# Kernel tuning notes

Measured on AMD Instinct MI355X. Metric: run time of the kernel, lower is better.

Reference implementation:

```python
import jax, jax.numpy as jnp
import numpy as np

L, H, P, R = 8192, 1024, 512, 256


def setup_inputs() -> dict:
    key = jax.random.key(0)
    ks = jax.random.split(key, 12)
    nrm = lambda k, s, std=0.01: std * jax.random.normal(k, s, dtype=jnp.float32)
    # Stable complex diagonal: |Lambda_bar| in [0.8, 0.999)
    mag = 0.8 + 0.199 * jax.random.uniform(ks[8], (P,), dtype=jnp.float32)
    phase = jnp.pi * jax.random.uniform(ks[9], (P,), dtype=jnp.float32)
    return {
        "input_sequence": jax.random.normal(ks[0], (L, H), dtype=jnp.float32),
        "F": nrm(ks[1], (R, H)),
        "H_proj": nrm(ks[2], (R, H)),
        "Delta_p": jnp.eye(R, dtype=jnp.float32),
        "Delta_r": jnp.eye(R, dtype=jnp.float32),
        "E": nrm(ks[3], (P, R)),
        "G": nrm(ks[4], (H, R)),
        "Lambda_bar_re": (mag * jnp.cos(phase)).astype(jnp.float32),
        "Lambda_bar_im": (mag * jnp.sin(phase)).astype(jnp.float32),
        "B_bar_re": nrm(ks[5], (P, H), 0.05),
        "B_bar_im": nrm(ks[6], (P, H), 0.05),
        "C_re": nrm(ks[7], (H, P), 0.05),
        "C_im": nrm(ks[10], (H, P), 0.05),
        "D": nrm(ks[11], (H, H), 0.02),
    }


def _binop(a, b):
    # Diagonal linear SSM associative combine: (lam, bu)
    return (b[0] * a[0], b[0] * a[1] + b[1])


def reference(input_sequence, F, H_proj, Delta_p, Delta_r, E, G,
              Lambda_bar_re, Lambda_bar_im, B_bar_re, B_bar_im,
              C_re, C_im, D):
    # p_k = Delta_p @ (F @ u_k), r_k = Delta_r @ (H_proj @ u_k)  -- vmapped over L via matmul
    p_seq = (input_sequence @ F.T) @ Delta_p.T            # (L, R)
    r_seq = (input_sequence @ H_proj.T) @ Delta_r.T       # (L, R)
    up_seq = jnp.concatenate([input_sequence, p_seq], axis=-1)  # (L, H+R)

    Lam = (Lambda_bar_re + 1j * Lambda_bar_im).astype(jnp.complex64)         # (P,)
    B_bar = (B_bar_re + 1j * B_bar_im).astype(jnp.complex64)                 # (P, H)
    B_ext = jnp.concatenate([B_bar, E.astype(jnp.complex64)], axis=1)        # (P, H+R)

    # Per-step driving term Bu_k = B_ext @ up_k
    Bu = up_seq.astype(jnp.complex64) @ B_ext.T                               # (L, P)
    Lam_el = jnp.broadcast_to(Lam, Bu.shape)                                  # (L, P)

    # Parallel associative scan: x_k = Lam * x_{k-1} + Bu_k
    _, xs = jax.lax.associative_scan(_binop, (Lam_el, Bu))                    # (L, P)

    C_tilde = (C_re + 1j * C_im).astype(jnp.complex64)                        # (H, P)
    # conj_sym=True branch: y_k = 2*Re(C_tilde @ x_k) + G @ r_k + D @ u_k
    y_seq = (2.0 * jnp.real(xs @ C_tilde.T)
             + r_seq @ G.T
             + input_sequence @ D.T)                                           # (L, H)
    return y_seq
```

## Files before the change

kernel.cpp:

```cpp
#include <hip/hip_runtime.h>
#include <stdint.h>

#define L_SEQ 8192
#define HDIM  1024
#define PDIM  512
#define RDIM  256
#define NCHUNK 64
#define CHUNK  128

typedef __attribute__((ext_vector_type(8))) short bf16x8;
typedef __attribute__((ext_vector_type(4))) float f32x4;
typedef __attribute__((ext_vector_type(4))) int   i32x4;

__device__ inline unsigned short f2bf(float x) {
  unsigned u = __builtin_bit_cast(unsigned, x);
  unsigned r = (u + 0x7fffu + ((u >> 16) & 1u)) >> 16;
  return (unsigned short)r;
}

__global__ __launch_bounds__(256) void transpose_cast(const float* __restrict__ src,
                                                      unsigned short* __restrict__ dst,
                                                      int R, int Hd) {
  __shared__ float tile[32][33];
  int bx = blockIdx.x * 32;
  int by = blockIdx.y * 32;
  int tx = threadIdx.x, ty = threadIdx.y;
#pragma unroll
  for (int dy = 0; dy < 32; dy += 8)
    tile[ty + dy][tx] = src[(size_t)(by + ty + dy) * Hd + bx + tx];
  __syncthreads();
#pragma unroll
  for (int dy = 0; dy < 32; dy += 8)
    dst[(size_t)(bx + ty + dy) * R + by + tx] = f2bf(tile[tx][ty + dy]);
}

__global__ __launch_bounds__(256) void cast_flat(const float* __restrict__ src,
                                                 unsigned short* __restrict__ dst,
                                                 int n4, float scale) {
  int g = blockIdx.x * 256 + threadIdx.x;
  if (g >= n4) return;
  float4 v = *(const float4*)(src + (size_t)g * 4);
  ushort4 o;
  o.x = f2bf(v.x * scale); o.y = f2bf(v.y * scale);
  o.z = f2bf(v.z * scale); o.w = f2bf(v.w * scale);
  *(ushort4*)(dst + (size_t)g * 4) = o;
}

__global__ __launch_bounds__(256) void cast_strided(const float* __restrict__ src, int ldsrc,
                                                    unsigned short* __restrict__ dst, int lddst,
                                                    int rows, int cols, float scale) {
  int g = blockIdx.x * 256 + threadIdx.x;
  int c4 = cols >> 2;
  int total = rows * c4;
  if (g >= total) return;
  int row = g / c4;
  int c = (g - row * c4) * 4;
  float4 v = *(const float4*)(src + (size_t)row * ldsrc + c);
  ushort4 o;
  o.x = f2bf(v.x * scale); o.y = f2bf(v.y * scale);
  o.z = f2bf(v.z * scale); o.w = f2bf(v.w * scale);
  *(ushort4*)(dst + (size_t)row * lddst + c) = o;
}

template <int HAS_ADD, int OUT_F32, int OUT_BF16>
__global__ __launch_bounds__(256) void gemm_bt(const unsigned short* __restrict__ A, int lda,
                                               const unsigned short* __restrict__ B, int ldb,
                                               float* __restrict__ C, int ldc,
                                               unsigned short* __restrict__ Cb, int ldcb,
                                               const float* __restrict__ Add, int ldadd,
                                               int K) {
  __shared__ __align__(16) unsigned short sA[128 * 32];
  __shared__ __align__(16) unsigned short sB[128 * 32];
  const int m0 = blockIdx.x * 128, n0 = blockIdx.y * 128;
  const int tid = threadIdx.x;
  const int lane = tid & 63, wave = tid >> 6;
  const int wm = wave >> 1, wn = wave & 1;
  const int frow = lane & 15, fg = lane >> 4;

  f32x4 acc[4][4] = {};

  for (int kt = 0; kt < K; kt += 32) {
    i32x4 ra[2], rb[2];
#pragma unroll
    for (int it = 0; it < 2; ++it) {
      int flat = it * 256 + tid;
      int r = flat >> 2, c8 = (flat & 3) * 8;
      ra[it] = *(const i32x4*)(A + (size_t)(m0 + r) * lda + kt + c8);
      rb[it] = *(const i32x4*)(B + (size_t)(n0 + r) * ldb + kt + c8);
    }
    __syncthreads();
#pragma unroll
    for (int it = 0; it < 2; ++it) {
      int flat = it * 256 + tid;
      int r = flat >> 2, c8 = (flat & 3) * 8;
      *(i32x4*)(sA + r * 32 + c8) = ra[it];
      *(i32x4*)(sB + r * 32 + c8) = rb[it];
    }
    __syncthreads();
    bf16x8 fa[4], fb[4];
#pragma unroll
    for (int f = 0; f < 4; ++f) {
      fa[f] = *(const bf16x8*)(sA + (wm * 64 + f * 16 + frow) * 32 + fg * 8);
      fb[f] = *(const bf16x8*)(sB + (wn * 64 + f * 16 + frow) * 32 + fg * 8);
    }
#pragma unroll
    for (int i = 0; i < 4; ++i)
#pragma unroll
      for (int j = 0; j < 4; ++j)
        acc[i][j] = __builtin_amdgcn_mfma_f32_16x16x32_bf16(fa[i], fb[j], acc[i][j], 0, 0, 0);
  }

  const int crow4 = (lane >> 4) * 4, ccol = lane & 15;
#pragma unroll
  for (int i = 0; i < 4; ++i)
#pragma unroll
    for (int j = 0; j < 4; ++j)
#pragma unroll
      for (int q = 0; q < 4; ++q) {
        int r = m0 + wm * 64 + i * 16 + crow4 + q;
        int c = n0 + wn * 64 + j * 16 + ccol;
        float v = acc[i][j][q];
        if (HAS_ADD) v += Add[(size_t)r * ldadd + c];
        if (OUT_F32) C[(size_t)r * ldc + c] = v;
        if (OUT_BF16) Cb[(size_t)r * ldcb + c] = f2bf(v);
      }
}

__global__ __launch_bounds__(256) void scan_carry(const float* __restrict__ Bu,
                                                  const float* __restrict__ lre,
                                                  const float* __restrict__ lim,
                                                  float* __restrict__ carry) {
  int g = blockIdx.x * 256 + threadIdx.x;
  int p = g & 511, c = g >> 9;
  float ar = lre[p], ai = lim[p];
  float sr = 0.f, si = 0.f;
  const float* base = Bu + (size_t)c * CHUNK * 1024 + p;
#pragma unroll 4
  for (int i = 0; i < CHUNK; ++i) {
    float br = base[(size_t)i * 1024];
    float bi = base[(size_t)i * 1024 + 512];
    float nr = ar * sr - ai * si + br;
    float ni = ar * si + ai * sr + bi;
    sr = nr; si = ni;
  }
  carry[c * 512 + p] = sr;
  carry[NCHUNK * 512 + c * 512 + p] = si;
}

__global__ __launch_bounds__(512) void scan_prefix(const float* __restrict__ carry,
                                                   const float* __restrict__ lre,
                                                   const float* __restrict__ lim,
                                                   float* __restrict__ prefix) {
  int p = threadIdx.x;
  float ar = lre[p], ai = lim[p];
  float cr = ar, ci = ai;
#pragma unroll
  for (int s = 0; s < 7; ++s) {
    float t = cr * cr - ci * ci;
    ci = 2.f * cr * ci;
    cr = t;
  }
  float sr = 0.f, si = 0.f;
  for (int c = 0; c < NCHUNK; ++c) {
    float br = carry[c * 512 + p], bi = carry[NCHUNK * 512 + c * 512 + p];
    float nr = cr * sr - ci * si + br;
    float ni = cr * si + ci * sr + bi;
    sr = nr; si = ni;
    prefix[c * 512 + p] = sr;
    prefix[NCHUNK * 512 + c * 512 + p] = si;
  }
}

__global__ __launch_bounds__(256) void scan_apply(const float* __restrict__ Bu,
                                                  const float* __restrict__ lre,
                                                  const float* __restrict__ lim,
                                                  const float* __restrict__ prefix,
                                                  unsigned short* __restrict__ A2) {
  int g = blockIdx.x * 256 + threadIdx.x;
  int p = g & 511, c = g >> 9;
  float ar = lre[p], ai = lim[p];
  float sr = 0.f, si = 0.f;
  if (c > 0) {
    sr = prefix[(c - 1) * 512 + p];
    si = prefix[NCHUNK * 512 + (c - 1) * 512 + p];
  }
  const float* base = Bu + (size_t)c * CHUNK * 1024 + p;
  unsigned short* ob = A2 + (size_t)c * CHUNK * 2048 + 1024 + p;
#pragma unroll 4
  for (int i = 0; i < CHUNK; ++i) {
    float br = base[(size_t)i * 1024];
    float bi = base[(size_t)i * 1024 + 512];
    float nr = ar * sr - ai * si + br;
    float ni = ar * si + ai * sr + bi;
    sr = nr; si = ni;
    ob[(size_t)i * 2048] = f2bf(sr);
    ob[(size_t)i * 2048 + 512] = f2bf(si);
  }
}

extern "C" void kernel_launch(void* const* d_in, const int* in_sizes, int n_in,
                              void* d_out, int out_size, void* d_ws, size_t ws_size,
                              hipStream_t stream) {
  const float* u   = (const float*)d_in[0];
  const float* F   = (const float*)d_in[1];
  const float* Hp  = (const float*)d_in[2];
  const float* dP  = (const float*)d_in[3];
  const float* dR  = (const float*)d_in[4];
  const float* E   = (const float*)d_in[5];
  const float* G   = (const float*)d_in[6];
  const float* lre = (const float*)d_in[7];
  const float* lim = (const float*)d_in[8];
  const float* Bre = (const float*)d_in[9];
  const float* Bim = (const float*)d_in[10];
  const float* Cre = (const float*)d_in[11];
  const float* Cim = (const float*)d_in[12];
  const float* Dm  = (const float*)d_in[13];
  float* y = (float*)d_out;

  uint8_t* ws = (uint8_t*)d_ws;
  size_t off = 0;
  auto alloc = [&](size_t bytes) {
    void* p = ws + off;
    off += (bytes + 255) & ~(size_t)255;
    return p;
  };
  unsigned short* A2  = (unsigned short*)alloc((size_t)L_SEQ * 2048 * 2);
  unsigned short* W1  = (unsigned short*)alloc((size_t)1024 * 1024 * 2);
  unsigned short* Wy  = (unsigned short*)alloc((size_t)1024 * 2048 * 2);
  float*          Bu  = (float*)alloc((size_t)L_SEQ * 1024 * 4);
  unsigned short* Ft  = (unsigned short*)alloc((size_t)1024 * 256 * 2);
  unsigned short* Ht  = (unsigned short*)alloc((size_t)1024 * 256 * 2);
  unsigned short* FpT = (unsigned short*)alloc((size_t)1024 * 256 * 2);
  unsigned short* HrT = (unsigned short*)alloc((size_t)1024 * 256 * 2);
  unsigned short* dPb = (unsigned short*)alloc((size_t)256 * 256 * 2);
  unsigned short* dRb = (unsigned short*)alloc((size_t)256 * 256 * 2);
  unsigned short* Eb  = (unsigned short*)alloc((size_t)512 * 256 * 2);
  unsigned short* Gb  = (unsigned short*)alloc((size_t)1024 * 256 * 2);
  float* carry  = (float*)alloc((size_t)2 * NCHUNK * 512 * 4);
  float* prefix = (float*)alloc((size_t)2 * NCHUNK * 512 * 4);
  (void)ws_size; (void)in_sizes; (void)n_in; (void)out_size;

  transpose_cast<<<dim3(32, 8), dim3(32, 8), 0, stream>>>(F, Ft, 256, 1024);
  transpose_cast<<<dim3(32, 8), dim3(32, 8), 0, stream>>>(Hp, Ht, 256, 1024);
  cast_flat<<<(65536 / 4 + 255) / 256, 256, 0, stream>>>(dP, dPb, 65536 / 4, 1.f);
  cast_flat<<<(65536 / 4 + 255) / 256, 256, 0, stream>>>(dR, dRb, 65536 / 4, 1.f);
  cast_flat<<<(131072 / 4 + 255) / 256, 256, 0, stream>>>(E, Eb, 131072 / 4, 1.f);
  cast_flat<<<(262144 / 4 + 255) / 256, 256, 0, stream>>>(G, Gb, 262144 / 4, 1.f);
  cast_strided<<<((L_SEQ * 256) + 255) / 256, 256, 0, stream>>>(u, 1024, A2, 2048, L_SEQ, 1024, 1.f);
  cast_flat<<<((512 * 1024 / 4) + 255) / 256, 256, 0, stream>>>(Bim, W1 + (size_t)512 * 1024, 512 * 1024 / 4, 1.f);
  cast_strided<<<((1024 * 128) + 255) / 256, 256, 0, stream>>>(Cre, 512, Wy + 1024, 2048, 1024, 512, 2.f);
  cast_strided<<<((1024 * 128) + 255) / 256, 256, 0, stream>>>(Cim, 512, Wy + 1536, 2048, 1024, 512, -2.f);

  gemm_bt<0, 0, 1><<<dim3(8, 2), 256, 0, stream>>>(Ft, 256, dPb, 256, nullptr, 0, FpT, 256, nullptr, 0, 256);
  gemm_bt<0, 0, 1><<<dim3(8, 2), 256, 0, stream>>>(Ht, 256, dRb, 256, nullptr, 0, HrT, 256, nullptr, 0, 256);
  gemm_bt<1, 0, 1><<<dim3(4, 8), 256, 0, stream>>>(Eb, 256, FpT, 256, nullptr, 0, W1, 1024, Bre, 1024, 256);
  gemm_bt<1, 0, 1><<<dim3(8, 8), 256, 0, stream>>>(Gb, 256, HrT, 256, nullptr, 0, Wy, 2048, Dm, 1024, 256);

  gemm_bt<0, 1, 0><<<dim3(64, 8), 256, 0, stream>>>(A2, 2048, W1, 1024, Bu, 1024, nullptr, 0, nullptr, 0, 1024);

  scan_carry<<<128, 256, 0, stream>>>(Bu, lre, lim, carry);
  scan_prefix<<<1, 512, 0, stream>>>(carry, lre, lim, prefix);
  scan_apply<<<128, 256, 0, stream>>>(Bu, lre, lim, prefix, A2);

  gemm_bt<0, 1, 0><<<dim3(64, 8), 256, 0, stream>>>(A2, 2048, Wy, 2048, y, 1024, nullptr, 0, nullptr, 0, 2048);
}
```

Measured before the change: 286.9 us.

## Fuse prep casts into one kernel, batch small GEMMs, use direct global-to-LDS loads

All ten cast and transpose launches are merged into a single prep kernel, and the four small weight GEMMs are paired into two launches using a z-indexed dual-parameter kernel. The GEMM mainloop now loads tiles straight from global memory into LDS with global_load_lds instead of staging through registers. The scan carry and prefix buffers move to a per-channel interleaved float2 layout, and the prefix loop is batched. The goal is lower launch overhead and less register and LDS traffic. The cost is an uncoalesced strided transpose inside prep and a GEMM loop that still has no double buffering.

```diff
diff --git a/kernel.cpp b/kernel.cpp
--- a/kernel.cpp
+++ b/kernel.cpp
@@ -2,15 +2,11 @@
 #include <stdint.h>
 
 #define L_SEQ 8192
-#define HDIM  1024
-#define PDIM  512
-#define RDIM  256
 #define NCHUNK 64
 #define CHUNK  128
 
 typedef __attribute__((ext_vector_type(8))) short bf16x8;
 typedef __attribute__((ext_vector_type(4))) float f32x4;
-typedef __attribute__((ext_vector_type(4))) int   i32x4;
 
 __device__ inline unsigned short f2bf(float x) {
   unsigned u = __builtin_bit_cast(unsigned, x);
@@ -18,84 +14,114 @@
   return (unsigned short)r;
 }
 
-__global__ __launch_bounds__(256) void transpose_cast(const float* __restrict__ src,
-                                                      unsigned short* __restrict__ dst,
-                                                      int R, int Hd) {
-  __shared__ float tile[32][33];
-  int bx = blockIdx.x * 32;
-  int by = blockIdx.y * 32;
-  int tx = threadIdx.x, ty = threadIdx.y;
-#pragma unroll
-  for (int dy = 0; dy < 32; dy += 8)
-    tile[ty + dy][tx] = src[(size_t)(by + ty + dy) * Hd + bx + tx];
-  __syncthreads();
-#pragma unroll
-  for (int dy = 0; dy < 32; dy += 8)
-    dst[(size_t)(bx + ty + dy) * R + by + tx] = f2bf(tile[tx][ty + dy]);
-}
-
-__global__ __launch_bounds__(256) void cast_flat(const float* __restrict__ src,
-                                                 unsigned short* __restrict__ dst,
-                                                 int n4, float scale) {
-  int g = blockIdx.x * 256 + threadIdx.x;
-  if (g >= n4) return;
-  float4 v = *(const float4*)(src + (size_t)g * 4);
-  ushort4 o;
-  o.x = f2bf(v.x * scale); o.y = f2bf(v.y * scale);
-  o.z = f2bf(v.z * scale); o.w = f2bf(v.w * scale);
-  *(ushort4*)(dst + (size_t)g * 4) = o;
-}
-
-__global__ __launch_bounds__(256) void cast_strided(const float* __restrict__ src, int ldsrc,
-                                                    unsigned short* __restrict__ dst, int lddst,
-                                                    int rows, int cols, float scale) {
-  int g = blockIdx.x * 256 + threadIdx.x;
-  int c4 = cols >> 2;
-  int total = rows * c4;
-  if (g >= total) return;
-  int row = g / c4;
-  int c = (g - row * c4) * 4;
-  float4 v = *(const float4*)(src + (size_t)row * ldsrc + c);
-  ushort4 o;
-  o.x = f2bf(v.x * scale); o.y = f2bf(v.y * scale);
-  o.z = f2bf(v.z * scale); o.w = f2bf(v.w * scale);
-  *(ushort4*)(dst + (size_t)row * lddst + c) = o;
+#define GLD16(g, l)                                                            \
+  __builtin_amdgcn_global_load_lds(                                            \
+      (const __attribute__((address_space(1))) unsigned int*)(g),              \
+      (__attribute__((address_space(3))) unsigned int*)(l), 16, 0, 0)
+
+__global__ __launch_bounds__(256) void prep(
+    const float* __restrict__ F, const float* __restrict__ Hp,
+    const float* __restrict__ dP, const float* __restrict__ dR,
+    const float* __restrict__ E, const float* __restrict__ G,
+    const float* __restrict__ Bim, const float* __restrict__ Cre,
+    const float* __restrict__ Cim, const float* __restrict__ u,
+    unsigned short* __restrict__ Ft, unsigned short* __restrict__ Ht,
+    unsigned short* __restrict__ dPb, unsigned short* __restrict__ dRb,
+    unsigned short* __restrict__ Eb, unsigned short* __restrict__ Gb,
+    unsigned short* __restrict__ W1im, unsigned short* __restrict__ Wy,
+    unsigned short* __restrict__ A2) {
+  int q = blockIdx.x * 256 + threadIdx.x;
+  if (q < 65536) {
+    int e = q * 4, i = e >> 8, j = e & 255;
+    ushort4 o;
+    o.x = f2bf(F[(size_t)(j + 0) * 1024 + i]);
+    o.y = f2bf(F[(size_t)(j + 1) * 1024 + i]);
+    o.z = f2bf(F[(size_t)(j + 2) * 1024 + i]);
+    o.w = f2bf(F[(size_t)(j + 3) * 1024 + i]);
+    *(ushort4*)(Ft + e) = o;
+  } else if (q < 131072) {
+    int e = (q - 65536) * 4, i = e >> 8, j = e & 255;
+    ushort4 o;
+    o.x = f2bf(Hp[(size_t)(j + 0) * 1024 + i]);
+    o.y = f2bf(Hp[(size_t)(j + 1) * 1024 + i]);
+    o.z = f2bf(Hp[(size_t)(j + 2) * 1024 + i]);
+    o.w = f2bf(Hp[(size_t)(j + 3) * 1024 + i]);
+    *(ushort4*)(Ht + e) = o;
+  } else if (q < 147456) {
+    int e = (q - 131072) * 4;
+    float4 v = *(const float4*)(dP + e);
+    ushort4 o = {f2bf(v.x), f2bf(v.y), f2bf(v.z), f2bf(v.w)};
+    *(ushort4*)(dPb + e) = o;
+  } else if (q < 163840) {
+    int e = (q - 147456) * 4;
+    float4 v = *(const float4*)(dR + e);
+    ushort4 o = {f2bf(v.x), f2bf(v.y), f2bf(v.z), f2bf(v.w)};
+    *(ushort4*)(dRb + e) = o;
+  } else if (q < 196608) {
+    int e = (q - 163840) * 4;
+    float4 v = *(const float4*)(E + e);
+    ushort4 o = {f2bf(v.x), f2bf(v.y), f2bf(v.z), f2bf(v.w)};
+    *(ushort4*)(Eb + e) = o;
+  } else if (q < 262144) {
+    int e = (q - 196608) * 4;
+    float4 v = *(const float4*)(G + e);
+    ushort4 o = {f2bf(v.x), f2bf(v.y), f2bf(v.z), f2bf(v.w)};
+    *(ushort4*)(Gb + e) = o;
+  } else if (q < 393216) {
+    int e = (q - 262144) * 4;
+    float4 v = *(const float4*)(Bim + e);
+    ushort4 o = {f2bf(v.x), f2bf(v.y), f2bf(v.z), f2bf(v.w)};
+    *(ushort4*)(W1im + e) = o;
+  } else if (q < 524288) {
+    int e = (q - 393216) * 4, i = e >> 9, j = e & 511;
+    float4 v = *(const float4*)(Cre + (size_t)i * 512 + j);
+    ushort4 o = {f2bf(2.f * v.x), f2bf(2.f * v.y), f2bf(2.f * v.z), f2bf(2.f * v.w)};
+    *(ushort4*)(Wy + (size_t)i * 2048 + 1024 + j) = o;
+  } else if (q < 655360) {
+    int e = (q - 524288) * 4, i = e >> 9, j = e & 511;
+    float4 v = *(const float4*)(Cim + (size_t)i * 512 + j);
+    ushort4 o = {f2bf(-2.f * v.x), f2bf(-2.f * v.y), f2bf(-2.f * v.z), f2bf(-2.f * v.w)};
+    *(ushort4*)(Wy + (size_t)i * 2048 + 1536 + j) = o;
+  } else {
+    int e = (q - 655360) * 4, i = e >> 10, j = e & 1023;
+    float4 v = *(const float4*)(u + (size_t)i * 1024 + j);
+    ushort4 o = {f2bf(v.x), f2bf(v.y), f2bf(v.z), f2bf(v.w)};
+    *(ushort4*)(A2 + (size_t)i * 2048 + j) = o;
+  }
 }
 
 template <int HAS_ADD, int OUT_F32, int OUT_BF16>
-__global__ __launch_bounds__(256) void gemm_bt(const unsigned short* __restrict__ A, int lda,
-                                               const unsigned short* __restrict__ B, int ldb,
-                                               float* __restrict__ C, int ldc,
-                                               unsigned short* __restrict__ Cb, int ldcb,
-                                               const float* __restrict__ Add, int ldadd,
-                                               int K) {
-  __shared__ __align__(16) unsigned short sA[128 * 32];
-  __shared__ __align__(16) unsigned short sB[128 * 32];
-  const int m0 = blockIdx.x * 128, n0 = blockIdx.y * 128;
+__device__ __forceinline__ void gemm_body(
+    const unsigned short* __restrict__ A, int lda,
+    const unsigned short* __restrict__ B, int ldb,
+    float* __restrict__ C, int ldc,
+    unsigned short* __restrict__ Cb, int ldcb,
+    const float* __restrict__ Add, int ldadd, int K, int m0, int n0,
+    unsigned short* sA, unsigned short* sB) {
   const int tid = threadIdx.x;
   const int lane = tid & 63, wave = tid >> 6;
   const int wm = wave >> 1, wn = wave & 1;
   const int frow = lane & 15, fg = lane >> 4;
 
+  const int srow = lane >> 2;
+  const int scol = (lane & 3) * 8;
+  const unsigned short* gA0 = A + (size_t)(m0 + wave * 32 + srow) * lda + scol;
+  const unsigned short* gA1 = gA0 + (size_t)16 * lda;
+  const unsigned short* gB0 = B + (size_t)(n0 + wave * 32 + srow) * ldb + scol;
+  const unsigned short* gB1 = gB0 + (size_t)16 * ldb;
+  unsigned short* lA0 = sA + wave * 1024;
+  unsigned short* lA1 = lA0 + 512;
+  unsigned short* lB0 = sB + wave * 1024;
+  unsigned short* lB1 = lB0 + 512;
+
   f32x4 acc[4][4] = {};
 
   for (int kt = 0; kt < K; kt += 32) {
-    i32x4 ra[2], rb[2];
-#pragma unroll
-    for (int it = 0; it < 2; ++it) {
-      int flat = it * 256 + tid;
-      int r = flat >> 2, c8 = (flat & 3) * 8;
-      ra[it] = *(const i32x4*)(A + (size_t)(m0 + r) * lda + kt + c8);
-      rb[it] = *(const i32x4*)(B + (size_t)(n0 + r) * ldb + kt + c8);
-    }
     __syncthreads();
-#pragma unroll
-    for (int it = 0; it < 2; ++it) {
-      int flat = it * 256 + tid;
-      int r = flat >> 2, c8 = (flat & 3) * 8;
-      *(i32x4*)(sA + r * 32 + c8) = ra[it];
-      *(i32x4*)(sB + r * 32 + c8) = rb[it];
-    }
+    GLD16(gA0 + kt, lA0);
+    GLD16(gA1 + kt, lA1);
+    GLD16(gB0 + kt, lB0);
+    GLD16(gB1 + kt, lB1);
     __syncthreads();
     bf16x8 fa[4], fb[4];
 #pragma unroll
@@ -126,10 +152,44 @@
       }
 }
 
+template <int HAS_ADD, int OUT_F32, int OUT_BF16>
+__global__ __launch_bounds__(256) void gemm_bt(
+    const unsigned short* __restrict__ A, int lda,
+    const unsigned short* __restrict__ B, int ldb,
+    float* __restrict__ C, int ldc,
+    unsigned short* __restrict__ Cb, int ldcb,
+    const float* __restrict__ Add, int ldadd, int K) {
+  __shared__ __align__(16) unsigned short sA[128 * 32];
+  __shared__ __align__(16) unsigned short sB[128 * 32];
+  gemm_body<HAS_ADD, OUT_F32, OUT_BF16>(A, lda, B, ldb, C, ldc, Cb, ldcb, Add,
+                                        ldadd, K, blockIdx.x * 128,
+                                        blockIdx.y * 128, sA, sB);
+}
+
+struct GemmP {
+  const unsigned short* A; int lda;
+  const unsigned short* B; int ldb;
+  float* C; int ldc;
+  unsigned short* Cb; int ldcb;
+  const float* Add; int ldadd;
+  int K; int gx;
+};
+
+template <int HAS_ADD, int OUT_F32, int OUT_BF16>
+__global__ __launch_bounds__(256) void gemm_bt_dual(GemmP p0, GemmP p1) {
+  __shared__ __align__(16) unsigned short sA[128 * 32];
+  __shared__ __align__(16) unsigned short sB[128 * 32];
+  GemmP p = blockIdx.z ? p1 : p0;
+  if ((int)blockIdx.x >= p.gx) return;
+  gemm_body<HAS_ADD, OUT_F32, OUT_BF16>(p.A, p.lda, p.B, p.ldb, p.C, p.ldc,
+                                        p.Cb, p.ldcb, p.Add, p.ldadd, p.K,
+                                        blockIdx.x * 128, blockIdx.y * 128, sA, sB);
+}
+
 __global__ __launch_bounds__(256) void scan_carry(const float* __restrict__ Bu,
                                                   const float* __restrict__ lre,
                                                   const float* __restrict__ lim,
-                                                  float* __restrict__ carry) {
+                                                  float2* __restrict__ carry2) {
   int g = blockIdx.x * 256 + threadIdx.x;
   int p = g & 511, c = g >> 9;
   float ar = lre[p], ai = lim[p];
@@ -143,14 +203,13 @@
     float ni = ar * si + ai * sr + bi;
     sr = nr; si = ni;
   }
-  carry[c * 512 + p] = sr;
-  carry[NCHUNK * 512 + c * 512 + p] = si;
-}
-
-__global__ __launch_bounds__(512) void scan_prefix(const float* __restrict__ carry,
+  carry2[(size_t)p * NCHUNK + c] = make_float2(sr, si);
+}
+
+__global__ __launch_bounds__(512) void scan_prefix(const float2* __restrict__ carry2,
                                                    const float* __restrict__ lre,
                                                    const float* __restrict__ lim,
-                                                   float* __restrict__ prefix) {
+                                                   float2* __restrict__ prefix2) {
   int p = threadIdx.x;
   float ar = lre[p], ai = lim[p];
   float cr = ar, ci = ai;
@@ -161,28 +220,34 @@
     cr = t;
   }
   float sr = 0.f, si = 0.f;
-  for (int c = 0; c < NCHUNK; ++c) {
-    float br = carry[c * 512 + p], bi = carry[NCHUNK * 512 + c * 512 + p];
-    float nr = cr * sr - ci * si + br;
-    float ni = cr * si + ci * sr + bi;
-    sr = nr; si = ni;
-    prefix[c * 512 + p] = sr;
-    prefix[NCHUNK * 512 + c * 512 + p] = si;
+  const float2* cp = carry2 + (size_t)p * NCHUNK;
+  float2* pp = prefix2 + (size_t)p * NCHUNK;
+  for (int cb = 0; cb < NCHUNK; cb += 16) {
+    float2 cv[16];
+#pragma unroll
+    for (int i = 0; i < 16; ++i) cv[i] = cp[cb + i];
+#pragma unroll
+    for (int i = 0; i < 16; ++i) {
+      float nr = cr * sr - ci * si + cv[i].x;
+      float ni = cr * si + ci * sr + cv[i].y;
+      sr = nr; si = ni;
+      pp[cb + i] = make_float2(sr, si);
+    }
   }
 }
 
 __global__ __launch_bounds__(256) void scan_apply(const float* __restrict__ Bu,
                                                   const float* __restrict__ lre,
                                                   const float* __restrict__ lim,
-                                                  const float* __restrict__ prefix,
+                                                  const float2* __restrict__ prefix2,
                                                   unsigned short* __restrict__ A2) {
   int g = blockIdx.x * 256 + threadIdx.x;
   int p = g & 511, c = g >> 9;
   float ar = lre[p], ai = lim[p];
   float sr = 0.f, si = 0.f;
   if (c > 0) {
-    sr = prefix[(c - 1) * 512 + p];
-    si = prefix[NCHUNK * 512 + (c - 1) * 512 + p];
+    float2 pr = prefix2[(size_t)p * NCHUNK + c - 1];
+    sr = pr.x; si = pr.y;
   }
   const float* base = Bu + (size_t)c * CHUNK * 1024 + p;
   unsigned short* ob = A2 + (size_t)c * CHUNK * 2048 + 1024 + p;
@@ -236,31 +301,29 @@
   unsigned short* dRb = (unsigned short*)alloc((size_t)256 * 256 * 2);
   unsigned short* Eb  = (unsigned short*)alloc((size_t)512 * 256 * 2);
   unsigned short* Gb  = (unsigned short*)alloc((size_t)1024 * 256 * 2);
-  float* carry  = (float*)alloc((size_t)2 * NCHUNK * 512 * 4);
-  float* prefix = (float*)alloc((size_t)2 * NCHUNK * 512 * 4);
+  float* carry  = (float*)alloc((size_t)512 * NCHUNK * 8);
+  float* prefix = (float*)alloc((size_t)512 * NCHUNK * 8);
   (void)ws_size; (void)in_sizes; (void)n_in; (void)out_size;
 
-  transpose_cast<<<dim3(32, 8), dim3(32, 8), 0, stream>>>(F, Ft, 256, 1024);
-  transpose_cast<<<dim3(32, 8), dim3(32, 8), 0, stream>>>(Hp, Ht, 256, 1024);
-  cast_flat<<<(65536 / 4 + 255) / 256, 256, 0, stream>>>(dP, dPb, 65536 / 4, 1.f);
-  cast_flat<<<(65536 / 4 + 255) / 256, 256, 0, stream>>>(dR, dRb, 65536 / 4, 1.f);
-  cast_flat<<<(131072 / 4 + 255) / 256, 256, 0, stream>>>(E, Eb, 131072 / 4, 1.f);
-  cast_flat<<<(262144 / 4 + 255) / 256, 256, 0, stream>>>(G, Gb, 262144 / 4, 1.f);
-  cast_strided<<<((L_SEQ * 256) + 255) / 256, 256, 0, stream>>>(u, 1024, A2, 2048, L_SEQ, 1024, 1.f);
-  cast_flat<<<((512 * 1024 / 4) + 255) / 256, 256, 0, stream>>>(Bim, W1 + (size_t)512 * 1024, 512 * 1024 / 4, 1.f);
-  cast_strided<<<((1024 * 128) + 255) / 256, 256, 0, stream>>>(Cre, 512, Wy + 1024, 2048, 1024, 512, 2.f);
-  cast_strided<<<((1024 * 128) + 255) / 256, 256, 0, stream>>>(Cim, 512, Wy + 1536, 2048, 1024, 512, -2.f);
-
-  gemm_bt<0, 0, 1><<<dim3(8, 2), 256, 0, stream>>>(Ft, 256, dPb, 256, nullptr, 0, FpT, 256, nullptr, 0, 256);
-  gemm_bt<0, 0, 1><<<dim3(8, 2), 256, 0, stream>>>(Ht, 256, dRb, 256, nullptr, 0, HrT, 256, nullptr, 0, 256);
-  gemm_bt<1, 0, 1><<<dim3(4, 8), 256, 0, stream>>>(Eb, 256, FpT, 256, nullptr, 0, W1, 1024, Bre, 1024, 256);
-  gemm_bt<1, 0, 1><<<dim3(8, 8), 256, 0, stream>>>(Gb, 256, HrT, 256, nullptr, 0, Wy, 2048, Dm, 1024, 256);
-
-  gemm_bt<0, 1, 0><<<dim3(64, 8), 256, 0, stream>>>(A2, 2048, W1, 1024, Bu, 1024, nullptr, 0, nullptr, 0, 1024);
-
-  scan_carry<<<128, 256, 0, stream>>>(Bu, lre, lim, carry);
-  scan_prefix<<<1, 512, 0, stream>>>(carry, lre, lim, prefix);
-  scan_apply<<<128, 256, 0, stream>>>(Bu, lre, lim, prefix, A2);
-
-  gemm_bt<0, 1, 0><<<dim3(64, 8), 256, 0, stream>>>(A2, 2048, Wy, 2048, y, 1024, nullptr, 0, nullptr, 0, 2048);
-}
+  prep<<<10752, 256, 0, stream>>>(F, Hp, dP, dR, E, G, Bim, Cre, Cim, u,
+                                  Ft, Ht, dPb, dRb, Eb, Gb,
+                                  W1 + (size_t)512 * 1024, Wy, A2);
+
+  GemmP pa = {Ft, 256, dPb, 256, nullptr, 0, FpT, 256, nullptr, 0, 256, 8};
+  GemmP pb = {Ht, 256, dRb, 256, nullptr, 0, HrT, 256, nullptr, 0, 256, 8};
+  gemm_bt_dual<0, 0, 1><<<dim3(8, 2, 2), 256, 0, stream>>>(pa, pb);
+
+  GemmP pc = {Eb, 256, FpT, 256, nullptr, 0, W1, 1024, Bre, 1024, 256, 4};
+  GemmP pd = {Gb, 256, HrT, 256, nullptr, 0, Wy, 2048, Dm, 1024, 256, 8};
+  gemm_bt_dual<1, 0, 1><<<dim3(8, 8, 2), 256, 0, stream>>>(pc, pd);
+
+  gemm_bt<0, 1, 0><<<dim3(64, 8), 256, 0, stream>>>(A2, 2048, W1, 1024, Bu, 1024,
+                                                    nullptr, 0, nullptr, 0, 1024);
+
+  scan_carry<<<128, 256, 0, stream>>>(Bu, lre, lim, (float2*)carry);
+  scan_prefix<<<1, 512, 0, stream>>>((const float2*)carry, lre, lim, (float2*)prefix);
+  scan_apply<<<128, 256, 0, stream>>>(Bu, lre, lim, (const float2*)prefix, A2);
+
+  gemm_bt<0, 1, 0><<<dim3(64, 8), 256, 0, stream>>>(A2, 2048, Wy, 2048, y, 1024,
+                                                    nullptr, 0, nullptr, 0, 2048);
+}
```

New measurement: 270.6 us. -5.7%, faster.
